# Optimization experiments

Hardware: AMD Instinct MI355X
Metric: run time of the kernel (lower is better)

Reference implementation:

```python
import jax, jax.numpy as jnp
import numpy as np

PERTURBATION_SCALE = 0.01

def setup_inputs() -> dict:
    key = jax.random.key(0)
    k1, k2, k3 = jax.random.split(key, 3)
    theta = jax.random.normal(k1, (256, 512), dtype=jnp.float32)
    basis_eval = jax.random.normal(k2, (100000, 512), dtype=jnp.float32)
    noise = jax.random.normal(k3, (256, 512), dtype=jnp.float32)
    return {"theta": theta, "basis_eval": basis_eval, "noise": noise}

def reference(theta, basis_eval, noise):
    # phi: [N, K] functional evaluations
    phi_raw = basis_eval @ theta.T
    phi_perturbed = basis_eval @ (theta + noise * PERTURBATION_SCALE).T
    # sign-crossings between consecutive evaluation points: [N-1, K]
    crossings = (phi_raw[:-1] * phi_raw[1:] < 0).astype(theta.dtype)
    crossings_p = (phi_perturbed[:-1] * phi_perturbed[1:] < 0).astype(theta.dtype)
    persistence = crossings * crossings_p  # [N-1, K]
    # fused pairwise shared-persistence: Gram matrix [K, K]
    gram = persistence.T @ persistence
    K = theta.shape[0]
    iu, ju = jnp.triu_indices(K, k=1)  # row-major i<j == itertools.combinations order
    return gram[iu, ju]  # [K*(K-1)/2]
```

## Files before the change

### kernel.cpp

```cpp
#include <hip/hip_runtime.h>
#include <hip/hip_bf16.h>
#include <stdint.h>

#define KDIM    256
#define NWORDS  1564
#define NW      1563
#define GEMM_GRID 1564

typedef float  f32x4  __attribute__((ext_vector_type(4)));
typedef __bf16 bf16x8 __attribute__((ext_vector_type(8)));

__device__ __forceinline__ void gl_lds16(const void* g, void* l) {
    __builtin_amdgcn_global_load_lds(
        (const __attribute__((address_space(1))) unsigned int*)g,
        (__attribute__((address_space(3))) unsigned int*)l, 16, 0, 0);
}

__global__ void build_w(const float* __restrict__ theta,
                        const float* __restrict__ noise,
                        __bf16* __restrict__ Wt) {
    int idx = blockIdx.x * 256 + threadIdx.x;
    int j = idx >> 9;
    int d = idx & 511;
    float v;
    if (j < KDIM) v = theta[j * 512 + d];
    else          v = theta[(j - KDIM) * 512 + d] + 0.01f * noise[(j - KDIM) * 512 + d];
    int t  = d >> 5;
    int g  = (d >> 3) & 3;
    int e  = d & 7;
    int gs = g ^ ((j >> 1) & 3);
    Wt[(((t << 9) + j) << 5) + (gs << 3) + e] = (__bf16)v;
}

__global__ void __launch_bounds__(512, 4)
gemm_signs(const float* __restrict__ basis,
           const __bf16* __restrict__ Wt,
           uint64_t* __restrict__ sbits) {
    __shared__ char smem[49152];

    const int tid    = threadIdx.x;
    const int lane   = tid & 63;
    const int wave   = tid >> 6;
    const int wr     = wave >> 2;
    const int wc     = wave & 3;
    const int lane16 = lane & 15;
    const int lgrp   = lane >> 4;

    const int orig = blockIdx.x;
    const int xcd  = orig & 7;
    const int wgid = (xcd < 4 ? xcd * 196 : 784 + (xcd - 4) * 195) + (orig >> 3);
    const int bn   = wgid & 1;
    const int bm   = wgid >> 1;

    const int ar = tid >> 2;
    const int ah = tid & 3;
    int arg = bm * 128 + ar; if (arg > 99999) arg = 99999;
    const float* abase_g = basis + (size_t)arg * 512 + ah * 8;
    const int awofs = ar * 64 + ((ah ^ (ar & 3)) << 4);

    const char* bpanel = (const char*)Wt + ((size_t)bn * 256 << 6) + wave * 2048 + lane * 16;
    auto stage_B = [&](int t) {
        char* bdst = smem + 16384 + ((t & 1) << 14) + wave * 2048;
        const char* src = bpanel + ((size_t)t << 15);
        gl_lds16(src,        bdst);
        gl_lds16(src + 1024, bdst + 1024);
    };

    f32x4  acc[4][4] = {};
    float4 ra[2][2];

    auto cvt_write_A = [&](int slot, int q) {
        bf16x8 a8;
        a8[0] = (__bf16)ra[slot][0].x; a8[1] = (__bf16)ra[slot][0].y;
        a8[2] = (__bf16)ra[slot][0].z; a8[3] = (__bf16)ra[slot][0].w;
        a8[4] = (__bf16)ra[slot][1].x; a8[5] = (__bf16)ra[slot][1].y;
        a8[6] = (__bf16)ra[slot][1].z; a8[7] = (__bf16)ra[slot][1].w;
        *(bf16x8*)(smem + (q << 13) + awofs) = a8;
    };

    ra[0][0] = *(const float4*)(abase_g);
    ra[0][1] = *(const float4*)(abase_g + 4);
    ra[1][0] = *(const float4*)(abase_g + 32);
    ra[1][1] = *(const float4*)(abase_g + 36);
    stage_B(0);
    asm volatile("s_waitcnt vmcnt(4)" ::: "memory");
    cvt_write_A(0, 0);
    asm volatile("s_waitcnt lgkmcnt(0)" ::: "memory");

    #pragma unroll
    for (int t = 0; t < 16; ++t) {
        if (t < 14) {
            ra[t & 1][0] = *(const float4*)(abase_g + (t + 2) * 32);
            ra[t & 1][1] = *(const float4*)(abase_g + (t + 2) * 32 + 4);
        }

        if (t < 14) asm volatile("s_waitcnt vmcnt(2)\ns_barrier" ::: "memory");
        else        asm volatile("s_waitcnt vmcnt(0)\ns_barrier" ::: "memory");

        if (t < 15) stage_B(t + 1);

        const char* ab = smem + ((t & 1) << 13);
        const char* bb = smem + 16384 + ((t & 1) << 14);

        bf16x8 bf[4];
        #pragma unroll
        for (int n = 0; n < 4; ++n) {
            int cc = wc * 64 + n * 16 + lane16;
            bf[n] = *(const bf16x8*)(bb + cc * 64 + ((lgrp ^ ((cc >> 1) & 3)) << 4));
        }
        bf16x8 af[4];
        #pragma unroll
        for (int m = 0; m < 4; ++m) {
            int rr = wr * 64 + m * 16 + lane16;
            af[m] = *(const bf16x8*)(ab + rr * 64 + ((lgrp ^ (rr & 3)) << 4));
        }
        asm volatile("s_waitcnt lgkmcnt(0)" ::: "memory");
        __builtin_amdgcn_sched_barrier(0);

        __builtin_amdgcn_s_setprio(1);
        #pragma unroll
        for (int m = 0; m < 4; ++m)
            #pragma unroll
            for (int n = 0; n < 4; ++n)
                acc[m][n] = __builtin_amdgcn_mfma_f32_16x16x32_bf16(
                    af[m], bf[n], acc[m][n], 0, 0, 0);
        __builtin_amdgcn_s_setprio(0);

        if (t < 15) {
            cvt_write_A((t + 1) & 1, (t + 1) & 1);
            asm volatile("s_waitcnt lgkmcnt(0)" ::: "memory");
        }
    }

    asm volatile("s_barrier" ::: "memory");
    unsigned char* sb = (unsigned char*)smem;
    #pragma unroll
    for (int m = 0; m < 4; ++m) {
        #pragma unroll
        for (int n = 0; n < 4; ++n) {
            int cc = wc * 64 + n * 16 + lane16;
            int rb = wr * 64 + m * 16 + lgrp * 4;
            uint32_t pk = 0;
            #pragma unroll
            for (int r = 0; r < 4; ++r)
                pk |= (acc[m][n][r] < 0.0f ? 1u : 0u) << (8 * r);
            *(uint32_t*)&sb[cc * 136 + rb] = pk;
        }
    }
    asm volatile("s_waitcnt lgkmcnt(0)\ns_barrier" ::: "memory");

    {
        const int col = tid & 255;
        const int wh  = tid >> 8;
        const unsigned char* src = &sb[col * 136 + wh * 64];
        uint64_t wbits = 0;
        #pragma unroll
        for (int k = 0; k < 16; ++k) {
            uint32_t qv = *(const uint32_t*)&src[4 * k];
            uint32_t p4 = ((qv & 0x01010101u) * 0x10204080u) >> 28;
            wbits |= (uint64_t)p4 << (4 * k);
        }
        sbits[(size_t)(bm * 2 + wh) * 512 + bn * 256 + col] = wbits;
    }
}

__global__ void crossing_masks(const uint64_t* __restrict__ sbits,
                               uint64_t* __restrict__ maskT) {
    const int w = blockIdx.x;
    const int j = threadIdx.x;
    uint64_t s0r = sbits[(size_t)w * 512 + j];
    uint64_t s0p = sbits[(size_t)w * 512 + 256 + j];
    uint64_t s1r = sbits[(size_t)(w + 1) * 512 + j];
    uint64_t s1p = sbits[(size_t)(w + 1) * 512 + 256 + j];
    uint64_t cr = s0r ^ ((s0r >> 1) | (s1r << 63));
    uint64_t cp = s0p ^ ((s0p >> 1) | (s1p << 63));
    uint64_t m = cr & cp;
    if (w == NW - 1) m &= 0x7FFFFFFFull;
    maskT[(size_t)w * 256 + j] = m;
}

__global__ void zero_out(float* __restrict__ out) {
    int i = blockIdx.x * 256 + threadIdx.x;
    if (i < 32640) out[i] = 0.0f;
}

__global__ void pair_popcount(const uint64_t* __restrict__ maskT,
                              float* __restrict__ out) {
    const int i = blockIdx.x;
    const int c = blockIdx.y;
    const int j = threadIdx.x;
    if (j <= i) return;
    int w0 = c * 196;
    int w1 = w0 + 196; if (w1 > NW) w1 = NW;
    uint32_t sum = 0;
    #pragma unroll 4
    for (int w = w0; w < w1; ++w) {
        uint64_t mi = maskT[(size_t)w * 256 + i];
        uint64_t mj = maskT[(size_t)w * 256 + j];
        sum += (uint32_t)__popcll(mi & mj);
    }
    const size_t idx = (size_t)i * (2 * KDIM - i - 1) / 2 + (size_t)(j - i - 1);
    atomicAdd(&out[idx], (float)sum);
}

extern "C" void kernel_launch(void* const* d_in, const int* in_sizes, int n_in,
                              void* d_out, int out_size, void* d_ws, size_t ws_size,
                              hipStream_t stream) {
    const float* theta = (const float*)d_in[0];
    const float* basis = (const float*)d_in[1];
    const float* noise = (const float*)d_in[2];
    float* out = (float*)d_out;

    char* ws = (char*)d_ws;
    __bf16*   Wt    = (__bf16*)ws;
    uint64_t* sbits = (uint64_t*)(ws + 524288);
    uint64_t* maskT = (uint64_t*)(ws + 524288 + (size_t)NWORDS * 512 * 8);

    hipLaunchKernelGGL(build_w,        dim3(1024),     dim3(256), 0, stream, theta, noise, Wt);
    hipLaunchKernelGGL(gemm_signs,     dim3(GEMM_GRID),dim3(512), 0, stream, basis, Wt, sbits);
    hipLaunchKernelGGL(crossing_masks, dim3(NW),       dim3(256), 0, stream, sbits, maskT);
    hipLaunchKernelGGL(zero_out,       dim3(128),      dim3(256), 0, stream, out);
    hipLaunchKernelGGL(pair_popcount,  dim3(KDIM, 8),  dim3(256), 0, stream, maskT, out);
}
```

Baseline: 122.3 us.

## Retile GEMM to 64-row blocks with all 512 columns and register-resident B

The sign GEMM is retiled so each workgroup covers 64 basis rows across all 512 weight columns (raw and perturbed), instead of 128 rows by 256 columns. Each wave now owns 64 columns and loads its B fragments straight from global memory into registers, double-buffered, so B no longer goes through LDS. Only A is staged in a smaller swizzled LDS buffer. This removes the LDS traffic and barriers for B and halves the A rows per block. The trade-off is uncached per-wave global reads of B, and every block rereads the full W panel, so B global traffic roughly doubles.

```diff
diff --git a/kernel.cpp b/kernel.cpp
--- a/kernel.cpp
+++ b/kernel.cpp
@@ -5,16 +5,10 @@
 #define KDIM    256
 #define NWORDS  1564
 #define NW      1563
-#define GEMM_GRID 1564
 
 typedef float  f32x4  __attribute__((ext_vector_type(4)));
 typedef __bf16 bf16x8 __attribute__((ext_vector_type(8)));
-
-__device__ __forceinline__ void gl_lds16(const void* g, void* l) {
-    __builtin_amdgcn_global_load_lds(
-        (const __attribute__((address_space(1))) unsigned int*)g,
-        (__attribute__((address_space(3))) unsigned int*)l, 16, 0, 0);
-}
+typedef __bf16 bf16x4 __attribute__((ext_vector_type(4)));
 
 __global__ void build_w(const float* __restrict__ theta,
                         const float* __restrict__ noise,
@@ -25,134 +19,117 @@
     float v;
     if (j < KDIM) v = theta[j * 512 + d];
     else          v = theta[(j - KDIM) * 512 + d] + 0.01f * noise[(j - KDIM) * 512 + d];
-    int t  = d >> 5;
-    int g  = (d >> 3) & 3;
-    int e  = d & 7;
-    int gs = g ^ ((j >> 1) & 3);
-    Wt[(((t << 9) + j) << 5) + (gs << 3) + e] = (__bf16)v;
+    Wt[((d >> 5) * 512 + j) * 32 + (d & 31)] = (__bf16)v;
 }
 
 __global__ void __launch_bounds__(512, 4)
 gemm_signs(const float* __restrict__ basis,
            const __bf16* __restrict__ Wt,
            uint64_t* __restrict__ sbits) {
-    __shared__ char smem[49152];
+    __shared__ char smem[34816];
 
     const int tid    = threadIdx.x;
     const int lane   = tid & 63;
-    const int wave   = tid >> 6;
-    const int wr     = wave >> 2;
-    const int wc     = wave & 3;
+    const int wc     = tid >> 6;
     const int lane16 = lane & 15;
     const int lgrp   = lane >> 4;
 
     const int orig = blockIdx.x;
-    const int xcd  = orig & 7;
-    const int wgid = (xcd < 4 ? xcd * 196 : 784 + (xcd - 4) * 195) + (orig >> 3);
-    const int bn   = wgid & 1;
-    const int bm   = wgid >> 1;
-
-    const int ar = tid >> 2;
-    const int ah = tid & 3;
-    int arg = bm * 128 + ar; if (arg > 99999) arg = 99999;
-    const float* abase_g = basis + (size_t)arg * 512 + ah * 8;
-    const int awofs = ar * 64 + ((ah ^ (ar & 3)) << 4);
-
-    const char* bpanel = (const char*)Wt + ((size_t)bn * 256 << 6) + wave * 2048 + lane * 16;
-    auto stage_B = [&](int t) {
-        char* bdst = smem + 16384 + ((t & 1) << 14) + wave * 2048;
-        const char* src = bpanel + ((size_t)t << 15);
-        gl_lds16(src,        bdst);
-        gl_lds16(src + 1024, bdst + 1024);
-    };
+    const int x    = orig & 7;
+    const int bm   = (x < 4 ? x * 196 : 784 + (x - 4) * 195) + (orig >> 3);
+
+    const int rl  = tid >> 3;
+    const int oct = tid & 7;
+    int r = bm * 64 + rl; if (r > 99999) r = 99999;
+    const float* asrc = basis + (size_t)r * 512 + oct * 4;
+    const int awofs = rl * 64 + (((oct >> 1) ^ ((rl >> 1) & 3)) << 4) + ((oct & 1) << 3);
+
+    const char* wbase = (const char*)Wt;
+    int bfofs[4];
+    #pragma unroll
+    for (int n = 0; n < 4; ++n)
+        bfofs[n] = (wc * 64 + n * 16 + lane16) * 64 + lgrp * 16;
 
     f32x4  acc[4][4] = {};
-    float4 ra[2][2];
-
-    auto cvt_write_A = [&](int slot, int q) {
-        bf16x8 a8;
-        a8[0] = (__bf16)ra[slot][0].x; a8[1] = (__bf16)ra[slot][0].y;
-        a8[2] = (__bf16)ra[slot][0].z; a8[3] = (__bf16)ra[slot][0].w;
-        a8[4] = (__bf16)ra[slot][1].x; a8[5] = (__bf16)ra[slot][1].y;
-        a8[6] = (__bf16)ra[slot][1].z; a8[7] = (__bf16)ra[slot][1].w;
-        *(bf16x8*)(smem + (q << 13) + awofs) = a8;
-    };
-
-    ra[0][0] = *(const float4*)(abase_g);
-    ra[0][1] = *(const float4*)(abase_g + 4);
-    ra[1][0] = *(const float4*)(abase_g + 32);
-    ra[1][1] = *(const float4*)(abase_g + 36);
-    stage_B(0);
-    asm volatile("s_waitcnt vmcnt(4)" ::: "memory");
-    cvt_write_A(0, 0);
+    float4 ra[2];
+    bf16x8 bf[2][4];
+
+    ra[0] = *(const float4*)(asrc);
+    ra[1] = *(const float4*)(asrc + 32);
+    #pragma unroll
+    for (int n = 0; n < 4; ++n)
+        bf[0][n] = *(const bf16x8*)(wbase + bfofs[n]);
+    {
+        bf16x4 v;
+        v[0] = (__bf16)ra[0].x; v[1] = (__bf16)ra[0].y;
+        v[2] = (__bf16)ra[0].z; v[3] = (__bf16)ra[0].w;
+        *(bf16x4*)(smem + awofs) = v;
+    }
     asm volatile("s_waitcnt lgkmcnt(0)" ::: "memory");
 
     #pragma unroll
     for (int t = 0; t < 16; ++t) {
-        if (t < 14) {
-            ra[t & 1][0] = *(const float4*)(abase_g + (t + 2) * 32);
-            ra[t & 1][1] = *(const float4*)(abase_g + (t + 2) * 32 + 4);
-        }
-
-        if (t < 14) asm volatile("s_waitcnt vmcnt(2)\ns_barrier" ::: "memory");
-        else        asm volatile("s_waitcnt vmcnt(0)\ns_barrier" ::: "memory");
-
-        if (t < 15) stage_B(t + 1);
-
-        const char* ab = smem + ((t & 1) << 13);
-        const char* bb = smem + 16384 + ((t & 1) << 14);
-
-        bf16x8 bf[4];
+        if (t < 14) ra[t & 1] = *(const float4*)(asrc + (t + 2) * 32);
+        if (t < 15) {
+            #pragma unroll
+            for (int n = 0; n < 4; ++n)
+                bf[(t + 1) & 1][n] =
+                    *(const bf16x8*)(wbase + (size_t)(t + 1) * 32768 + bfofs[n]);
+        }
+
+        __builtin_amdgcn_s_barrier();
+
+        if (t < 15) {
+            bf16x4 v;
+            float4 rv = ra[(t + 1) & 1];
+            v[0] = (__bf16)rv.x; v[1] = (__bf16)rv.y;
+            v[2] = (__bf16)rv.z; v[3] = (__bf16)rv.w;
+            *(bf16x4*)(smem + (((t + 1) & 1) << 12) + awofs) = v;
+        }
+
+        const char* ab = smem + ((t & 1) << 12);
         #pragma unroll
-        for (int n = 0; n < 4; ++n) {
-            int cc = wc * 64 + n * 16 + lane16;
-            bf[n] = *(const bf16x8*)(bb + cc * 64 + ((lgrp ^ ((cc >> 1) & 3)) << 4));
-        }
-        bf16x8 af[4];
-        #pragma unroll
-        for (int m = 0; m < 4; ++m) {
-            int rr = wr * 64 + m * 16 + lane16;
-            af[m] = *(const bf16x8*)(ab + rr * 64 + ((lgrp ^ (rr & 3)) << 4));
-        }
-        asm volatile("s_waitcnt lgkmcnt(0)" ::: "memory");
-        __builtin_amdgcn_sched_barrier(0);
-
-        __builtin_amdgcn_s_setprio(1);
-        #pragma unroll
-        for (int m = 0; m < 4; ++m)
-            #pragma unroll
-            for (int n = 0; n < 4; ++n)
-                acc[m][n] = __builtin_amdgcn_mfma_f32_16x16x32_bf16(
-                    af[m], bf[n], acc[m][n], 0, 0, 0);
-        __builtin_amdgcn_s_setprio(0);
-
-        if (t < 15) {
-            cvt_write_A((t + 1) & 1, (t + 1) & 1);
+        for (int mh = 0; mh < 2; ++mh) {
+            bf16x8 af[2];
+            #pragma unroll
+            for (int mi = 0; mi < 2; ++mi) {
+                int rr = (mh * 2 + mi) * 16 + lane16;
+                af[mi] = *(const bf16x8*)(ab + rr * 64
+                           + ((lgrp ^ ((rr >> 1) & 3)) << 4));
+            }
             asm volatile("s_waitcnt lgkmcnt(0)" ::: "memory");
-        }
-    }
-
-    asm volatile("s_barrier" ::: "memory");
+            __builtin_amdgcn_sched_barrier(0);
+            __builtin_amdgcn_s_setprio(1);
+            #pragma unroll
+            for (int mi = 0; mi < 2; ++mi)
+                #pragma unroll
+                for (int n = 0; n < 4; ++n)
+                    acc[mh * 2 + mi][n] = __builtin_amdgcn_mfma_f32_16x16x32_bf16(
+                        af[mi], bf[t & 1][n], acc[mh * 2 + mi][n], 0, 0, 0);
+            __builtin_amdgcn_s_setprio(0);
+        }
+    }
+
+    __builtin_amdgcn_s_barrier();
     unsigned char* sb = (unsigned char*)smem;
     #pragma unroll
     for (int m = 0; m < 4; ++m) {
         #pragma unroll
         for (int n = 0; n < 4; ++n) {
             int cc = wc * 64 + n * 16 + lane16;
-            int rb = wr * 64 + m * 16 + lgrp * 4;
+            int rb = m * 16 + lgrp * 4;
             uint32_t pk = 0;
             #pragma unroll
-            for (int r = 0; r < 4; ++r)
-                pk |= (acc[m][n][r] < 0.0f ? 1u : 0u) << (8 * r);
-            *(uint32_t*)&sb[cc * 136 + rb] = pk;
-        }
-    }
-    asm volatile("s_waitcnt lgkmcnt(0)\ns_barrier" ::: "memory");
+            for (int rg = 0; rg < 4; ++rg)
+                pk |= (acc[m][n][rg] < 0.0f ? 1u : 0u) << (8 * rg);
+            *(uint32_t*)&sb[cc * 68 + rb] = pk;
+        }
+    }
+    asm volatile("s_waitcnt lgkmcnt(0)" ::: "memory");
+    __builtin_amdgcn_s_barrier();
 
     {
-        const int col = tid & 255;
-        const int wh  = tid >> 8;
-        const unsigned char* src = &sb[col * 136 + wh * 64];
+        const unsigned char* src = &sb[tid * 68];
         uint64_t wbits = 0;
         #pragma unroll
         for (int k = 0; k < 16; ++k) {
@@ -160,7 +137,7 @@
             uint32_t p4 = ((qv & 0x01010101u) * 0x10204080u) >> 28;
             wbits |= (uint64_t)p4 << (4 * k);
         }
-        sbits[(size_t)(bm * 2 + wh) * 512 + bn * 256 + col] = wbits;
+        sbits[(size_t)bm * 512 + tid] = wbits;
     }
 }
 
@@ -216,9 +193,9 @@
     uint64_t* sbits = (uint64_t*)(ws + 524288);
     uint64_t* maskT = (uint64_t*)(ws + 524288 + (size_t)NWORDS * 512 * 8);
 
-    hipLaunchKernelGGL(build_w,        dim3(1024),     dim3(256), 0, stream, theta, noise, Wt);
-    hipLaunchKernelGGL(gemm_signs,     dim3(GEMM_GRID),dim3(512), 0, stream, basis, Wt, sbits);
-    hipLaunchKernelGGL(crossing_masks, dim3(NW),       dim3(256), 0, stream, sbits, maskT);
-    hipLaunchKernelGGL(zero_out,       dim3(128),      dim3(256), 0, stream, out);
-    hipLaunchKernelGGL(pair_popcount,  dim3(KDIM, 8),  dim3(256), 0, stream, maskT, out);
-}
+    hipLaunchKernelGGL(build_w,        dim3(1024),    dim3(256), 0, stream, theta, noise, Wt);
+    hipLaunchKernelGGL(gemm_signs,     dim3(NWORDS),  dim3(512), 0, stream, basis, Wt, sbits);
+    hipLaunchKernelGGL(crossing_masks, dim3(NW),      dim3(256), 0, stream, sbits, maskT);
+    hipLaunchKernelGGL(zero_out,       dim3(128),     dim3(256), 0, stream, out);
+    hipLaunchKernelGGL(pair_popcount,  dim3(KDIM, 8), dim3(256), 0, stream, maskT, out);
+}
```

After: 122.5 us. About the same (+0.2%).
